# Kernel optimization log

Measured on AMD Instinct MI355X. Metric: run time of the kernel, lower is better.

Reference implementation:

```python
import math
import jax, jax.numpy as jnp
import numpy as np

PROB_SPARSE_FACTOR = 0.4


def setup_inputs() -> dict:
    key = jax.random.key(0)
    kq, kk, kv = jax.random.split(key, 3)
    B, H, T, S, D = 2, 16, 2048, 2048, 64
    q = jax.random.normal(kq, (B, H, T, D), dtype=jnp.float32)
    k = jax.random.normal(kk, (B, H, S, D), dtype=jnp.float32)
    v = jax.random.normal(kv, (B, H, S, D), dtype=jnp.float32)
    return {"q": q, "k": k, "v": v}


def reference(q, k, v):
    B, H, T, D = q.shape
    S = k.shape[2]
    scaling = 1.0 / math.sqrt(D)
    # Informer-style top-u query count (static, derived from shapes)
    u = max(int(min(PROB_SPARSE_FACTOR * math.log(S), T * 0.5)), int(T * 0.3))

    # KLD scoring over full attention approximation: [B,H,T,S]
    attn_approx = jnp.einsum("bhtd,bhsd->bhts", q * scaling, k)
    attn_approx = jnp.clip(attn_approx, -50.0, 50.0)
    attn_approx = attn_approx - jnp.max(attn_approx, axis=-1, keepdims=True)
    sm = jax.nn.softmax(attn_approx, axis=-1)
    log_uniform = math.log(S)
    kl_score = jnp.sum(sm * (jnp.log(sm + 1e-10) + log_uniform), axis=-1)  # [B,H,T]

    # Select top-u most informative queries per (b,h)
    _, topk_idx = jax.lax.top_k(kl_score, u)  # [B,H,u]

    # Sparse attention only for selected queries
    q_red = jnp.take_along_axis(q, topk_idx[..., None], axis=2)  # [B,H,u,D]
    scores = jnp.einsum("bhud,bhsd->bhus", q_red, k) * scaling
    scores = jnp.clip(scores, -50.0, 50.0)
    scores = scores - jnp.max(scores, axis=-1, keepdims=True)
    w = jax.nn.softmax(scores, axis=-1)
    w = jnp.clip(w, 1e-9, 1.0)
    out_red = jnp.einsum("bhus,bhsd->bhud", w, v)  # [B,H,u,D]

    # Scatter reduced outputs back into a zero-initialized full output
    b_i = jnp.arange(B)[:, None, None]
    h_i = jnp.arange(H)[None, :, None]
    out = jnp.zeros_like(q).at[b_i, h_i, topk_idx].set(out_red)
    return out
```

## Files before the change

### kernel.cpp

```cpp
#include <hip/hip_runtime.h>
#include <math.h>

#define T_DIM 2048
#define S_DIM 2048
#define D_DIM 64
#define BH_DIM 32
#define U_SEL 614
#define LOG_S_D 7.624618986159398
#define LOG2E_F 1.4426950408889634f
#define LN2_D 0.6931471805599453
#define SCL_Q (0.125f * LOG2E_F)

typedef __attribute__((ext_vector_type(8))) short bf16x8;
typedef __attribute__((ext_vector_type(4))) short bf16x4;
typedef __attribute__((ext_vector_type(4))) float f32x4;

__device__ __forceinline__ unsigned short bf16_rne(float x) {
  unsigned u = __float_as_uint(x);
  u += 0x7FFF + ((u >> 16) & 1);
  return (unsigned short)(u >> 16);
}
__device__ __forceinline__ float bf16_to_f(unsigned short h) {
  return __uint_as_float(((unsigned)h) << 16);
}

#define GLD_LDS16(g, l)                                                        \
  __builtin_amdgcn_global_load_lds(                                            \
      (const __attribute__((address_space(1))) unsigned int*)(const void*)(g), \
      (__attribute__((address_space(3))) unsigned int*)(void*)(l), 16, 0, 0)

__device__ __forceinline__ void stage_img16(const unsigned short* __restrict__ g,
                                            unsigned short* l, int lane, int w) {
#pragma unroll
  for (int it = 0; it < 4; ++it) {
    const int chunk = it * 4 + w;
    GLD_LDS16((const char*)g + chunk * 1024 + lane * 16, (char*)l + chunk * 1024);
  }
}
__device__ __forceinline__ void stage_img8(const unsigned short* __restrict__ g,
                                           unsigned short* l, int lane, int w) {
#pragma unroll
  for (int it = 0; it < 2; ++it) {
    const int chunk = it * 4 + w;
    GLD_LDS16((const char*)g + chunk * 1024 + lane * 16, (char*)l + chunk * 1024);
  }
}

__device__ __forceinline__ bf16x8 ldfrag_sw(const unsigned short* buf, int row, int chunk) {
  return *(const bf16x8*)(buf + (row << 6) + (((chunk) ^ (row & 7)) << 3));
}
__device__ __forceinline__ bf16x8 ldfrag_k128(const unsigned short* buf, int row, int chunk) {
  return *(const bf16x8*)(buf + ((row >> 6) << 12) + ((row & 63) << 6) +
                          (((chunk) ^ (row & 7)) << 3));
}

__global__ __launch_bounds__(256) void convert_kernel(
    const float* __restrict__ kin, const float* __restrict__ vin,
    unsigned short* __restrict__ kimg, unsigned short* __restrict__ vt_g,
    float* __restrict__ out) {
  __shared__ float vld[128][65];
  const int jb = blockIdx.x;
  const int tid = threadIdx.x;
  if (jb < 1024) {
    const int bh = jb >> 5, tl = jb & 31;
    const float* src = kin + ((size_t)bh * 2048 + tl * 64) * 64;
    unsigned short* dst = kimg + (size_t)(bh * 32 + tl) * 8192;
#pragma unroll
    for (int g = 0; g < 2; ++g) {
      const int flat = g * 256 + tid;
      const int r = flat >> 3, c = flat & 7;
      const float4 f0 = *(const float4*)(src + r * 64 + c * 8);
      const float4 f1 = *(const float4*)(src + r * 64 + c * 8 + 4);
      const float xs[8] = {f0.x, f0.y, f0.z, f0.w, f1.x, f1.y, f1.z, f1.w};
      bf16x8 hv, lv;
#pragma unroll
      for (int j = 0; j < 8; ++j) {
        const unsigned short h = bf16_rne(xs[j]);
        hv[j] = (short)h;
        lv[j] = (short)bf16_rne(xs[j] - bf16_to_f(h));
      }
      const int base = (r << 6) + ((c ^ (r & 7)) << 3);
      *(bf16x8*)(dst + base) = hv;
      *(bf16x8*)(dst + 4096 + base) = lv;
    }
  } else if (jb < 1536) {
    const int jv = jb - 1024;
    const int bh = jv >> 4, tl = jv & 15;
    const float* src = vin + ((size_t)bh * 2048 + tl * 128) * 64;
#pragma unroll
    for (int g = 0; g < 8; ++g) {
      const int f = g * 256 + tid;
      const int r = f >> 4, c4 = f & 15;
      const float4 x = *(const float4*)(src + r * 64 + c4 * 4);
      vld[r][c4 * 4 + 0] = x.x;
      vld[r][c4 * 4 + 1] = x.y;
      vld[r][c4 * 4 + 2] = x.z;
      vld[r][c4 * 4 + 3] = x.w;
    }
    __syncthreads();
    unsigned short* dst = vt_g + (size_t)(bh * 16 + tl) * 8192;
#pragma unroll
    for (int g = 0; g < 4; ++g) {
      const int oc = g * 256 + tid;
      const int d = oc >> 4, cc = oc & 15;
      bf16x8 hv;
#pragma unroll
      for (int j = 0; j < 8; ++j) hv[j] = (short)bf16_rne(vld[cc * 8 + j][d]);
      *(bf16x8*)(dst + (d << 7) + (((cc ^ (d & 15))) << 3)) = hv;
    }
  } else {
    float4* o4 = (float4*)out;
    const size_t b = (size_t)(jb - 1536);
#pragma unroll
    for (int g = 0; g < 8; ++g)
      o4[b * 2048 + g * 256 + tid] = make_float4(0.f, 0.f, 0.f, 0.f);
  }
}

__global__ __launch_bounds__(256, 4) void kl_score_mfma(
    const float* __restrict__ q, const unsigned short* __restrict__ kimg,
    float2* __restrict__ zw) {
  __shared__ __align__(16) unsigned short lbuf[2][8192];
  const int b = blockIdx.x;
  const int bh = b & 31;
  const int t0 = ((b >> 5) & 15) * 128;
  const int shalf = b >> 9;
  const int tid = threadIdx.x;
  const int lane = tid & 63, w = tid >> 6, quad = lane >> 4, l15 = lane & 15;
  const float* qb = q + (size_t)bh * (2048 * 64) + (size_t)t0 * 64;
  const unsigned short* kb = kimg + (size_t)bh * (32 * 8192);
  const int tg0 = shalf * 16;

  {
#pragma unroll
    for (int g = 0; g < 4; ++g) {
      const int flat = g * 256 + tid;
      const int r = flat >> 3, c = flat & 7;
      const float4 f0 = *(const float4*)(qb + r * 64 + c * 8);
      const float4 f1 = *(const float4*)(qb + r * 64 + c * 8 + 4);
      const float xs[8] = {f0.x, f0.y, f0.z, f0.w, f1.x, f1.y, f1.z, f1.w};
      bf16x8 hv, lv;
#pragma unroll
      for (int j = 0; j < 8; ++j) {
        const float x = xs[j] * SCL_Q;
        const unsigned short h = bf16_rne(x);
        hv[j] = (short)h;
        lv[j] = (short)bf16_rne(x - bf16_to_f(h));
      }
      const int r2 = r & 63, hi2 = r >> 6;
      const int base = hi2 * 4096 + (r2 << 6) + ((c ^ (r2 & 7)) << 3);
      *(bf16x8*)(&lbuf[0][0] + base) = hv;
      *(bf16x8*)(&lbuf[1][0] + base) = lv;
    }
  }
  __syncthreads();

  bf16x8 ah[2][2], al[2][2];
#pragma unroll
  for (int rt = 0; rt < 2; ++rt) {
    const int row = w * 32 + rt * 16 + l15;
#pragma unroll
    for (int kc = 0; kc < 2; ++kc) {
      ah[rt][kc] = ldfrag_k128(&lbuf[0][0], row, kc * 4 + quad);
      al[rt][kc] = ldfrag_k128(&lbuf[1][0], row, kc * 4 + quad);
    }
  }
  __syncthreads();

  stage_img16(kb + (size_t)tg0 * 8192, &lbuf[0][0], lane, w);
  __syncthreads();

  float Zf[8], Wf[8];
#pragma unroll
  for (int i = 0; i < 8; ++i) { Zf[i] = 0.f; Wf[i] = 0.f; }

  for (int t = 0; t < 16; ++t) {
    if (t < 15)
      stage_img16(kb + (size_t)(tg0 + t + 1) * 8192, &lbuf[(t + 1) & 1][0], lane, w);
    const unsigned short* cb = &lbuf[t & 1][0];

    f32x4 acc[2][4];
#pragma unroll
    for (int rt = 0; rt < 2; ++rt)
#pragma unroll
      for (int ct = 0; ct < 4; ++ct) acc[rt][ct] = (f32x4){0.f, 0.f, 0.f, 0.f};

#pragma unroll
    for (int ct = 0; ct < 4; ++ct) {
      const int srow = ct * 16 + l15;
      const bf16x8 bh0 = ldfrag_sw(cb, srow, quad);
      const bf16x8 bl0 = ldfrag_sw(cb + 4096, srow, quad);
      const bf16x8 bh1 = ldfrag_sw(cb, srow, 4 + quad);
      const bf16x8 bl1 = ldfrag_sw(cb + 4096, srow, 4 + quad);
#pragma unroll
      for (int rt = 0; rt < 2; ++rt) {
        f32x4 c = acc[rt][ct];
        c = __builtin_amdgcn_mfma_f32_16x16x32_bf16(ah[rt][0], bh0, c, 0, 0, 0);
        c = __builtin_amdgcn_mfma_f32_16x16x32_bf16(al[rt][0], bh0, c, 0, 0, 0);
        c = __builtin_amdgcn_mfma_f32_16x16x32_bf16(ah[rt][0], bl0, c, 0, 0, 0);
        c = __builtin_amdgcn_mfma_f32_16x16x32_bf16(ah[rt][1], bh1, c, 0, 0, 0);
        c = __builtin_amdgcn_mfma_f32_16x16x32_bf16(al[rt][1], bh1, c, 0, 0, 0);
        c = __builtin_amdgcn_mfma_f32_16x16x32_bf16(ah[rt][1], bl1, c, 0, 0, 0);
        acc[rt][ct] = c;
      }
    }

#pragma unroll
    for (int rt = 0; rt < 2; ++rt)
#pragma unroll
      for (int r = 0; r < 4; ++r) {
        float zp = 0.f, wp = 0.f;
#pragma unroll
        for (int ct = 0; ct < 4; ++ct) {
          const float tt = acc[rt][ct][r];
          const float e = exp2f(tt);
          zp += e;
          wp = fmaf(e, tt, wp);
        }
        Zf[rt * 4 + r] += zp;
        Wf[rt * 4 + r] += wp;
      }
    __syncthreads();
  }

#pragma unroll
  for (int i = 0; i < 8; ++i) {
    float Zt = Zf[i], Wt = Wf[i];
#pragma unroll
    for (int mask = 1; mask <= 8; mask <<= 1) {
      Zt += __shfl_xor(Zt, mask);
      Wt += __shfl_xor(Wt, mask);
    }
    if (l15 == 0) {
      const int row = t0 + w * 32 + (i >> 2) * 16 + quad * 4 + (i & 3);
      zw[((size_t)shalf * 32 + bh) * 2048 + row] = make_float2(Zt, Wt);
    }
  }
}

__global__ __launch_bounds__(1024) void topk_kernel(const float2* __restrict__ zw,
                                                    int* __restrict__ topk) {
  __shared__ float sv[2048];
  __shared__ int si[2048];
  const int bh = blockIdx.x;
  const int tid = threadIdx.x;
  for (int i = tid; i < 2048; i += 1024) {
    const float2 a = zw[(size_t)bh * 2048 + i];
    const float2 c = zw[(size_t)(32 + bh) * 2048 + i];
    const double Z = (double)a.x + (double)c.x;
    const double W = (double)a.y + (double)c.y;
    sv[i] = (float)(LN2_D * (W / Z) - log(Z) + LOG_S_D);
    si[i] = i;
  }
  __syncthreads();
  for (int kk = 2; kk <= 2048; kk <<= 1) {
    for (int j = kk >> 1; j > 0; j >>= 1) {
      const int p = tid;
      const int i = ((p & ~(j - 1)) << 1) | (p & (j - 1));
      const int pr = i | j;
      const float v1 = sv[i], v2 = sv[pr];
      const int i1 = si[i], i2 = si[pr];
      const bool beforePI = (v2 > v1) || (v2 == v1 && i2 < i1);
      const bool dirDesc = ((i & kk) == 0);
      const bool doSwap = dirDesc ? beforePI : !beforePI;
      if (doSwap) { sv[i] = v2; sv[pr] = v1; si[i] = i2; si[pr] = i1; }
      __syncthreads();
    }
  }
  for (int i = tid; i < U_SEL; i += 1024) topk[bh * U_SEL + i] = si[i];
}

struct __align__(16) SmC {
  unsigned short qs[64 * 64];
  unsigned short kt[128 * 64];
  union { unsigned short vt[64 * 128]; float obuf[64 * 64]; } u;
  unsigned short ps[4][64 * 40];
  float zred[4][64];
};

__global__ __launch_bounds__(256, 3) void sparse_attn_mfma(
    const float* __restrict__ q, const unsigned short* __restrict__ kimg,
    const unsigned short* __restrict__ vt_g, const int* __restrict__ topk,
    float* __restrict__ out) {
  __shared__ SmC sm;
  const int b = blockIdx.x;
  const int bh = b & 31;
  const int l0 = (b >> 5) * 64;
  const int tid = threadIdx.x;
  const int lane = tid & 63, w = tid >> 6, quad = lane >> 4, l15 = lane & 15;
  const float* qb = q + (size_t)bh * (2048 * 64);
  const unsigned short* kb = kimg + (size_t)bh * (32 * 8192);
  const unsigned short* vtb = vt_g + (size_t)bh * (16 * 8192);
  const int* tkb = topk + bh * U_SEL;

  {
#pragma unroll
    for (int g = 0; g < 2; ++g) {
      const int ch = g * 256 + tid;
      const int r = ch >> 3, c = ch & 7;
      const int l = l0 + r;
      const int row = (l < U_SEL) ? tkb[l] : tkb[0];
      const float4 f0 = *(const float4*)(qb + (size_t)row * 64 + c * 8);
      const float4 f1 = *(const float4*)(qb + (size_t)row * 64 + c * 8 + 4);
      const float xs[8] = {f0.x, f0.y, f0.z, f0.w, f1.x, f1.y, f1.z, f1.w};
      bf16x8 hv;
#pragma unroll
      for (int j = 0; j < 8; ++j) hv[j] = (short)bf16_rne(xs[j] * SCL_Q);
      *(bf16x8*)&sm.qs[(r << 6) + ((c ^ (r & 7)) << 3)] = hv;
    }
  }
  stage_img8(kb, sm.kt, lane, w);
  stage_img8(kb + 8192, sm.kt + 4096, lane, w);
  stage_img16(vtb, sm.u.vt, lane, w);
  __syncthreads();

  bf16x8 qf[4][2];
#pragma unroll
  for (int nt = 0; nt < 4; ++nt)
#pragma unroll
    for (int kc = 0; kc < 2; ++kc)
      qf[nt][kc] = ldfrag_sw(sm.qs, nt * 16 + l15, kc * 4 + quad);

  float zrun[4] = {0.f, 0.f, 0.f, 0.f};
  f32x4 oacc[4][4];
#pragma unroll
  for (int a = 0; a < 4; ++a)
#pragma unroll
    for (int b2 = 0; b2 < 4; ++b2) oacc[a][b2] = (f32x4){0.f, 0.f, 0.f, 0.f};

  for (int st = 0; st < 16; ++st) {
    f32x4 sacc[2][4];
#pragma unroll
    for (int mt = 0; mt < 2; ++mt)
#pragma unroll
      for (int nt = 0; nt < 4; ++nt) sacc[mt][nt] = (f32x4){0.f, 0.f, 0.f, 0.f};
#pragma unroll
    for (int mt = 0; mt < 2; ++mt) {
      const int arow = w * 32 + mt * 16 + l15;
      const bf16x8 a0 = ldfrag_k128(sm.kt, arow, quad);
      const bf16x8 a1 = ldfrag_k128(sm.kt, arow, 4 + quad);
#pragma unroll
      for (int nt = 0; nt < 4; ++nt) {
        f32x4 c = sacc[mt][nt];
        c = __builtin_amdgcn_mfma_f32_16x16x32_bf16(a0, qf[nt][0], c, 0, 0, 0);
        c = __builtin_amdgcn_mfma_f32_16x16x32_bf16(a1, qf[nt][1], c, 0, 0, 0);
        sacc[mt][nt] = c;
      }
    }

#pragma unroll
    for (int nt = 0; nt < 4; ++nt) {
      float zl = 0.f;
#pragma unroll
      for (int mt = 0; mt < 2; ++mt) {
        bf16x4 pw;
#pragma unroll
        for (int r = 0; r < 4; ++r) {
          const float p = exp2f(sacc[mt][nt][r]);
          zl += p;
          pw[r] = (short)bf16_rne(p);
        }
        *(bf16x4*)&sm.ps[w][(nt * 16 + l15) * 40 + mt * 16 + quad * 4] = pw;
      }
      zrun[nt] += zl;
    }

    {
      bf16x8 vbf[4];
#pragma unroll
      for (int dt = 0; dt < 4; ++dt) {
        const int d = dt * 16 + l15;
        vbf[dt] = *(const bf16x8*)&sm.u.vt[(d << 7) + (((w * 4 + quad) ^ l15) << 3)];
      }
#pragma unroll
      for (int mtq = 0; mtq < 4; ++mtq) {
        const bf16x8 pa = *(const bf16x8*)&sm.ps[w][(mtq * 16 + l15) * 40 + quad * 8];
#pragma unroll
        for (int dt = 0; dt < 4; ++dt)
          oacc[mtq][dt] = __builtin_amdgcn_mfma_f32_16x16x32_bf16(pa, vbf[dt], oacc[mtq][dt], 0, 0, 0);
      }
    }
    __syncthreads();
    if (st < 15) {
      stage_img8(kb + (size_t)(2 * st + 2) * 8192, sm.kt, lane, w);
      stage_img8(kb + (size_t)(2 * st + 3) * 8192, sm.kt + 4096, lane, w);
      stage_img16(vtb + (size_t)(st + 1) * 8192, sm.u.vt, lane, w);
      __syncthreads();
    }
  }

#pragma unroll
  for (int nt = 0; nt < 4; ++nt) {
    float z = zrun[nt];
    z += __shfl_xor(z, 16);
    z += __shfl_xor(z, 32);
    if (quad == 0) sm.zred[w][nt * 16 + l15] = z;
  }
  for (int i = tid; i < 64 * 64; i += 256) sm.u.obuf[i] = 0.f;
  __syncthreads();
#pragma unroll
  for (int mtq = 0; mtq < 4; ++mtq)
#pragma unroll
    for (int r = 0; r < 4; ++r) {
      const int qr = mtq * 16 + quad * 4 + r;
#pragma unroll
      for (int dt = 0; dt < 4; ++dt)
        atomicAdd(&sm.u.obuf[qr * 64 + dt * 16 + l15], oacc[mtq][dt][r]);
    }
  __syncthreads();
  {
    const int qr = tid >> 2, seg = tid & 3;
    const int l = l0 + qr;
    if (l < U_SEL) {
      const float Zt = sm.zred[0][qr] + sm.zred[1][qr] + sm.zred[2][qr] + sm.zred[3][qr];
      const float inv = 1.0f / Zt;
      const int row = tkb[l];
      float* op = &out[((size_t)bh * T_DIM + row) * 64 + seg * 16];
      const float* ob = &sm.u.obuf[qr * 64 + seg * 16];
#pragma unroll
      for (int j = 0; j < 4; ++j) {
        float4 o;
        o.x = ob[j * 4 + 0] * inv;
        o.y = ob[j * 4 + 1] * inv;
        o.z = ob[j * 4 + 2] * inv;
        o.w = ob[j * 4 + 3] * inv;
        *(float4*)&op[j * 4] = o;
      }
    }
  }
}

extern "C" void kernel_launch(void* const* d_in, const int* in_sizes, int n_in,
                              void* d_out, int out_size, void* d_ws, size_t ws_size,
                              hipStream_t stream) {
  const float* q = (const float*)d_in[0];
  const float* k = (const float*)d_in[1];
  const float* v = (const float*)d_in[2];
  float* out = (float*)d_out;
  char* ws = (char*)d_ws;
  float2* zw = (float2*)ws;
  int* topk = (int*)(ws + 1048576);
  unsigned short* kimg = (unsigned short*)(ws + 1310720);
  unsigned short* vt_g = (unsigned short*)(ws + 18087936);

  convert_kernel<<<dim3(2048), dim3(256), 0, stream>>>(k, v, kimg, vt_g, out);
  kl_score_mfma<<<dim3(1024), dim3(256), 0, stream>>>(q, kimg, zw);
  topk_kernel<<<dim3(BH_DIM), dim3(1024), 0, stream>>>(zw, topk);
  sparse_attn_mfma<<<dim3(320), dim3(256), 0, stream>>>(q, kimg, vt_g, topk, out);
}
```

Baseline: 251.2 us.

## Split S dimension across blocks, replace bitonic sort with rank-count top-k

The KL-score kernel now splits the key dimension four ways and accumulates Z/W with float atomics into a workspace region that is zeroed up front. Top-k drops the shared-memory bitonic sort and has each thread compute its element's rank by linear comparison, with two blocks per head emitting winners through an atomic counter. Sparse attention splits S in two, doubling the grid, and a new merge kernel sums the partial outputs and normalisers before scattering. This adds parallelism for the small grids at the cost of atomics, an extra launch and partial-result traffic, and the atomic-counter top-k returns indices in nondeterministic order.

```diff
diff --git a/kernel.cpp b/kernel.cpp
--- a/kernel.cpp
+++ b/kernel.cpp
@@ -6,11 +6,20 @@
 #define D_DIM 64
 #define BH_DIM 32
 #define U_SEL 614
+#define LT_N 10
 #define LOG_S_D 7.624618986159398
 #define LOG2E_F 1.4426950408889634f
 #define LN2_D 0.6931471805599453
 #define SCL_Q (0.125f * LOG2E_F)
 
+#define WS_ZW 0u
+#define WS_CNT 1048576u
+#define WS_TOPK 1048704u
+#define WS_PO 1127424u
+#define WS_PZ 11613184u
+#define WS_KIMG 11777024u
+#define WS_VT 28554240u
+
 typedef __attribute__((ext_vector_type(8))) short bf16x8;
 typedef __attribute__((ext_vector_type(4))) short bf16x4;
 typedef __attribute__((ext_vector_type(4))) float f32x4;
@@ -57,7 +66,7 @@
 __global__ __launch_bounds__(256) void convert_kernel(
     const float* __restrict__ kin, const float* __restrict__ vin,
     unsigned short* __restrict__ kimg, unsigned short* __restrict__ vt_g,
-    float* __restrict__ out) {
+    float* __restrict__ out, float4* __restrict__ wszero) {
   __shared__ float vld[128][65];
   const int jb = blockIdx.x;
   const int tid = threadIdx.x;
@@ -108,12 +117,18 @@
       for (int j = 0; j < 8; ++j) hv[j] = (short)bf16_rne(vld[cc * 8 + j][d]);
       *(bf16x8*)(dst + (d << 7) + (((cc ^ (d & 15))) << 3)) = hv;
     }
-  } else {
+  } else if (jb < 2048) {
     float4* o4 = (float4*)out;
     const size_t b = (size_t)(jb - 1536);
 #pragma unroll
     for (int g = 0; g < 8; ++g)
       o4[b * 2048 + g * 256 + tid] = make_float4(0.f, 0.f, 0.f, 0.f);
+  } else {
+#pragma unroll
+    for (int g = 0; g < 16; ++g) {
+      const unsigned i = (unsigned)(jb - 2048) * 4096u + g * 256u + tid;
+      if (i < 65544u) wszero[i] = make_float4(0.f, 0.f, 0.f, 0.f);
+    }
   }
 }
 
@@ -124,12 +139,12 @@
   const int b = blockIdx.x;
   const int bh = b & 31;
   const int t0 = ((b >> 5) & 15) * 128;
-  const int shalf = b >> 9;
+  const int sq = b >> 9;
   const int tid = threadIdx.x;
   const int lane = tid & 63, w = tid >> 6, quad = lane >> 4, l15 = lane & 15;
   const float* qb = q + (size_t)bh * (2048 * 64) + (size_t)t0 * 64;
   const unsigned short* kb = kimg + (size_t)bh * (32 * 8192);
-  const int tg0 = shalf * 16;
+  const int tg0 = sq * 8;
 
   {
 #pragma unroll
@@ -174,8 +189,8 @@
 #pragma unroll
   for (int i = 0; i < 8; ++i) { Zf[i] = 0.f; Wf[i] = 0.f; }
 
-  for (int t = 0; t < 16; ++t) {
-    if (t < 15)
+  for (int t = 0; t < 8; ++t) {
+    if (t < 7)
       stage_img16(kb + (size_t)(tg0 + t + 1) * 8192, &lbuf[(t + 1) & 1][0], lane, w);
     const unsigned short* cb = &lbuf[t & 1][0];
 
@@ -233,59 +248,60 @@
     }
     if (l15 == 0) {
       const int row = t0 + w * 32 + (i >> 2) * 16 + quad * 4 + (i & 3);
-      zw[((size_t)shalf * 32 + bh) * 2048 + row] = make_float2(Zt, Wt);
+      float2* p = &zw[(size_t)bh * 2048 + row];
+      atomicAdd(&p->x, Zt);
+      atomicAdd(&p->y, Wt);
     }
   }
 }
 
 __global__ __launch_bounds__(1024) void topk_kernel(const float2* __restrict__ zw,
-                                                    int* __restrict__ topk) {
-  __shared__ float sv[2048];
-  __shared__ int si[2048];
-  const int bh = blockIdx.x;
+                                                    int* __restrict__ topk,
+                                                    int* __restrict__ cnt) {
+  __shared__ __align__(16) float sv[2048];
+  const int bh = blockIdx.x >> 1;
+  const int half = blockIdx.x & 1;
   const int tid = threadIdx.x;
   for (int i = tid; i < 2048; i += 1024) {
-    const float2 a = zw[(size_t)bh * 2048 + i];
-    const float2 c = zw[(size_t)(32 + bh) * 2048 + i];
-    const double Z = (double)a.x + (double)c.x;
-    const double W = (double)a.y + (double)c.y;
+    const float2 f = zw[(size_t)bh * 2048 + i];
+    const double Z = (double)f.x, W = (double)f.y;
     sv[i] = (float)(LN2_D * (W / Z) - log(Z) + LOG_S_D);
-    si[i] = i;
-  }
-  __syncthreads();
-  for (int kk = 2; kk <= 2048; kk <<= 1) {
-    for (int j = kk >> 1; j > 0; j >>= 1) {
-      const int p = tid;
-      const int i = ((p & ~(j - 1)) << 1) | (p & (j - 1));
-      const int pr = i | j;
-      const float v1 = sv[i], v2 = sv[pr];
-      const int i1 = si[i], i2 = si[pr];
-      const bool beforePI = (v2 > v1) || (v2 == v1 && i2 < i1);
-      const bool dirDesc = ((i & kk) == 0);
-      const bool doSwap = dirDesc ? beforePI : !beforePI;
-      if (doSwap) { sv[i] = v2; sv[pr] = v1; si[i] = i2; si[pr] = i1; }
-      __syncthreads();
-    }
-  }
-  for (int i = tid; i < U_SEL; i += 1024) topk[bh * U_SEL + i] = si[i];
+  }
+  __syncthreads();
+  const int e = half * 1024 + tid;
+  const float v = sv[e];
+  int r = 0;
+  for (int j = 0; j < 2048; j += 4) {
+    const float4 x = *(const float4*)&sv[j];
+    r += (x.x > v) || (x.x == v && (j + 0) < e);
+    r += (x.y > v) || (x.y == v && (j + 1) < e);
+    r += (x.z > v) || (x.z == v && (j + 2) < e);
+    r += (x.w > v) || (x.w == v && (j + 3) < e);
+  }
+  if (r < U_SEL) topk[bh * U_SEL + atomicAdd(&cnt[bh], 1)] = e;
 }
 
 struct __align__(16) SmC {
   unsigned short qs[64 * 64];
-  unsigned short kt[128 * 64];
-  union { unsigned short vt[64 * 128]; float obuf[64 * 64]; } u;
+  union {
+    struct { unsigned short kt[128 * 64]; unsigned short vt[64 * 128]; } s;
+    float obuf[64 * 64];
+  } u;
   unsigned short ps[4][64 * 40];
   float zred[4][64];
 };
 
-__global__ __launch_bounds__(256, 3) void sparse_attn_mfma(
+__global__ __launch_bounds__(256, 2) void sparse_attn_mfma(
     const float* __restrict__ q, const unsigned short* __restrict__ kimg,
     const unsigned short* __restrict__ vt_g, const int* __restrict__ topk,
-    float* __restrict__ out) {
+    float* __restrict__ po2, float* __restrict__ pz2) {
   __shared__ SmC sm;
   const int b = blockIdx.x;
   const int bh = b & 31;
-  const int l0 = (b >> 5) * 64;
+  const int rest = b >> 5;
+  const int lt = rest % LT_N;
+  const int sh = rest / LT_N;
+  const int l0 = lt * 64;
   const int tid = threadIdx.x;
   const int lane = tid & 63, w = tid >> 6, quad = lane >> 4, l15 = lane & 15;
   const float* qb = q + (size_t)bh * (2048 * 64);
@@ -309,9 +325,9 @@
       *(bf16x8*)&sm.qs[(r << 6) + ((c ^ (r & 7)) << 3)] = hv;
     }
   }
-  stage_img8(kb, sm.kt, lane, w);
-  stage_img8(kb + 8192, sm.kt + 4096, lane, w);
-  stage_img16(vtb, sm.u.vt, lane, w);
+  stage_img8(kb + (size_t)(sh * 16) * 8192, sm.u.s.kt, lane, w);
+  stage_img8(kb + (size_t)(sh * 16 + 1) * 8192, sm.u.s.kt + 4096, lane, w);
+  stage_img16(vtb + (size_t)(sh * 8) * 8192, sm.u.s.vt, lane, w);
   __syncthreads();
 
   bf16x8 qf[4][2];
@@ -328,25 +344,20 @@
 #pragma unroll
     for (int b2 = 0; b2 < 4; ++b2) oacc[a][b2] = (f32x4){0.f, 0.f, 0.f, 0.f};
 
-  for (int st = 0; st < 16; ++st) {
+  for (int st = 0; st < 8; ++st) {
     f32x4 sacc[2][4];
 #pragma unroll
     for (int mt = 0; mt < 2; ++mt)
 #pragma unroll
-      for (int nt = 0; nt < 4; ++nt) sacc[mt][nt] = (f32x4){0.f, 0.f, 0.f, 0.f};
-#pragma unroll
-    for (int mt = 0; mt < 2; ++mt) {
-      const int arow = w * 32 + mt * 16 + l15;
-      const bf16x8 a0 = ldfrag_k128(sm.kt, arow, quad);
-      const bf16x8 a1 = ldfrag_k128(sm.kt, arow, 4 + quad);
-#pragma unroll
       for (int nt = 0; nt < 4; ++nt) {
-        f32x4 c = sacc[mt][nt];
+        const int arow = w * 32 + mt * 16 + l15;
+        const bf16x8 a0 = ldfrag_k128(sm.u.s.kt, arow, quad);
+        const bf16x8 a1 = ldfrag_k128(sm.u.s.kt, arow, 4 + quad);
+        f32x4 c = (f32x4){0.f, 0.f, 0.f, 0.f};
         c = __builtin_amdgcn_mfma_f32_16x16x32_bf16(a0, qf[nt][0], c, 0, 0, 0);
         c = __builtin_amdgcn_mfma_f32_16x16x32_bf16(a1, qf[nt][1], c, 0, 0, 0);
         sacc[mt][nt] = c;
       }
-    }
 
 #pragma unroll
     for (int nt = 0; nt < 4; ++nt) {
@@ -367,10 +378,11 @@
 
     {
       bf16x8 vbf[4];
+      const int cc = w * 4 + quad;
 #pragma unroll
       for (int dt = 0; dt < 4; ++dt) {
         const int d = dt * 16 + l15;
-        vbf[dt] = *(const bf16x8*)&sm.u.vt[(d << 7) + (((w * 4 + quad) ^ l15) << 3)];
+        vbf[dt] = *(const bf16x8*)&sm.u.s.vt[(d << 7) + ((cc ^ (d & 15)) << 3)];
       }
 #pragma unroll
       for (int mtq = 0; mtq < 4; ++mtq) {
@@ -381,10 +393,10 @@
       }
     }
     __syncthreads();
-    if (st < 15) {
-      stage_img8(kb + (size_t)(2 * st + 2) * 8192, sm.kt, lane, w);
-      stage_img8(kb + (size_t)(2 * st + 3) * 8192, sm.kt + 4096, lane, w);
-      stage_img16(vtb + (size_t)(st + 1) * 8192, sm.u.vt, lane, w);
+    if (st < 7) {
+      stage_img8(kb + (size_t)(sh * 16 + 2 * st + 2) * 8192, sm.u.s.kt, lane, w);
+      stage_img8(kb + (size_t)(sh * 16 + 2 * st + 3) * 8192, sm.u.s.kt + 4096, lane, w);
+      stage_img16(vtb + (size_t)(sh * 8 + st + 1) * 8192, sm.u.s.vt, lane, w);
       __syncthreads();
     }
   }
@@ -396,6 +408,7 @@
     z += __shfl_xor(z, 32);
     if (quad == 0) sm.zred[w][nt * 16 + l15] = z;
   }
+  __syncthreads();
   for (int i = tid; i < 64 * 64; i += 256) sm.u.obuf[i] = 0.f;
   __syncthreads();
 #pragma unroll
@@ -409,23 +422,46 @@
     }
   __syncthreads();
   {
-    const int qr = tid >> 2, seg = tid & 3;
-    const int l = l0 + qr;
+    const int base = (bh * LT_N + lt) * 2 + sh;
+    float4* po4 = (float4*)(po2 + (size_t)base * 4096);
+    const float4* ob4 = (const float4*)sm.u.obuf;
+#pragma unroll
+    for (int g = 0; g < 4; ++g) po4[g * 256 + tid] = ob4[g * 256 + tid];
+    if (tid < 64)
+      pz2[(size_t)base * 64 + tid] =
+          sm.zred[0][tid] + sm.zred[1][tid] + sm.zred[2][tid] + sm.zred[3][tid];
+  }
+}
+
+__global__ __launch_bounds__(256) void merge_kernel(
+    const float* __restrict__ po2, const float* __restrict__ pz2,
+    const int* __restrict__ topk, float* __restrict__ out) {
+  __shared__ float zs[64];
+  const int b = blockIdx.x;
+  const int bh = b & 31;
+  const int lt = b >> 5;
+  const int tid = threadIdx.x;
+  const int base = (bh * LT_N + lt) * 2;
+  const float4* p0 = (const float4*)(po2 + (size_t)base * 4096);
+  const float4* p1 = (const float4*)(po2 + (size_t)(base + 1) * 4096);
+  const int* tkb = topk + bh * U_SEL;
+  if (tid < 64) zs[tid] = pz2[(size_t)base * 64 + tid] + pz2[(size_t)(base + 1) * 64 + tid];
+  __syncthreads();
+#pragma unroll
+  for (int g = 0; g < 4; ++g) {
+    const int i = g * 256 + tid;
+    const int qr = i >> 4;
+    const int l = lt * 64 + qr;
     if (l < U_SEL) {
-      const float Zt = sm.zred[0][qr] + sm.zred[1][qr] + sm.zred[2][qr] + sm.zred[3][qr];
-      const float inv = 1.0f / Zt;
       const int row = tkb[l];
-      float* op = &out[((size_t)bh * T_DIM + row) * 64 + seg * 16];
-      const float* ob = &sm.u.obuf[qr * 64 + seg * 16];
-#pragma unroll
-      for (int j = 0; j < 4; ++j) {
-        float4 o;
-        o.x = ob[j * 4 + 0] * inv;
-        o.y = ob[j * 4 + 1] * inv;
-        o.z = ob[j * 4 + 2] * inv;
-        o.w = ob[j * 4 + 3] * inv;
-        *(float4*)&op[j * 4] = o;
-      }
+      const float inv = 1.0f / zs[qr];
+      const float4 a = p0[i], c = p1[i];
+      float4 o;
+      o.x = (a.x + c.x) * inv;
+      o.y = (a.y + c.y) * inv;
+      o.z = (a.z + c.z) * inv;
+      o.w = (a.w + c.w) * inv;
+      ((float4*)out)[((size_t)bh * 2048 + row) * 16 + (i & 15)] = o;
     }
   }
 }
@@ -438,13 +474,17 @@
   const float* v = (const float*)d_in[2];
   float* out = (float*)d_out;
   char* ws = (char*)d_ws;
-  float2* zw = (float2*)ws;
-  int* topk = (int*)(ws + 1048576);
-  unsigned short* kimg = (unsigned short*)(ws + 1310720);
-  unsigned short* vt_g = (unsigned short*)(ws + 18087936);
-
-  convert_kernel<<<dim3(2048), dim3(256), 0, stream>>>(k, v, kimg, vt_g, out);
-  kl_score_mfma<<<dim3(1024), dim3(256), 0, stream>>>(q, kimg, zw);
-  topk_kernel<<<dim3(BH_DIM), dim3(1024), 0, stream>>>(zw, topk);
-  sparse_attn_mfma<<<dim3(320), dim3(256), 0, stream>>>(q, kimg, vt_g, topk, out);
-}
+  float2* zw = (float2*)(ws + WS_ZW);
+  int* cnt = (int*)(ws + WS_CNT);
+  int* topk = (int*)(ws + WS_TOPK);
+  float* po2 = (float*)(ws + WS_PO);
+  float* pz2 = (float*)(ws + WS_PZ);
+  unsigned short* kimg = (unsigned short*)(ws + WS_KIMG);
+  unsigned short* vt_g = (unsigned short*)(ws + WS_VT);
+
+  convert_kernel<<<dim3(2065), dim3(256), 0, stream>>>(k, v, kimg, vt_g, out, (float4*)ws);
+  kl_score_mfma<<<dim3(2048), dim3(256), 0, stream>>>(q, kimg, zw);
+  topk_kernel<<<dim3(64), dim3(1024), 0, stream>>>(zw, topk, cnt);
+  sparse_attn_mfma<<<dim3(640), dim3(256), 0, stream>>>(q, kimg, vt_g, topk, po2, pz2);
+  merge_kernel<<<dim3(320), dim3(256), 0, stream>>>(po2, pz2, topk, out);
+}
```

New measurement: 903.0 us. +259.4%, slower.
